# Performance work log

Measured on AMD Instinct MI355X. Metric: run time of the kernel, lower is better.

## Reference

```python
import jax, jax.numpy as jnp
from jax import lax
import numpy as np

BIG = jnp.float32(1e6)  # 'no feature in this column' sentinel distance


def setup_inputs() -> dict:
    key = jax.random.key(0)
    k1, k2 = jax.random.split(key)
    # Binary segmentation masks in {0,1}; surf() only uses astype(bool), i.e. != 0.
    pred = (jax.random.uniform(k1, (512, 512)) > 0.5).astype(jnp.float32)
    gt = (jax.random.uniform(k2, (512, 512)) > 0.5).astype(jnp.float32)
    return {"pred": pred, "gt": gt}


def _erode(x):
    # scipy binary_erosion with connectivity-1 (cross) structure, border_value=0:
    # pixel survives iff it and its 4 neighbors are all True (out-of-bounds = False).
    p = jnp.pad(x, 1, constant_values=False)
    return x & p[:-2, 1:-1] & p[2:, 1:-1] & p[1:-1, :-2] & p[1:-1, 2:]


def _edt(feat):
    # Exact Euclidean distance from every pixel to the nearest True pixel of `feat`.
    # Equals scipy distance_transform_edt(~feat) in the original code.
    H, W = feat.shape
    # --- pass 1: per-column 1D distance |r - k| to nearest feature (two sweeps) ---
    def sweep(carry, row):
        c = jnp.where(row, jnp.float32(0.0), carry + jnp.float32(1.0))
        return c, c
    init = jnp.full((W,), BIG, dtype=jnp.float32)
    _, df = lax.scan(sweep, init, feat)          # distance to nearest feature above
    _, db = lax.scan(sweep, init, feat[::-1])    # ... below
    g = jnp.minimum(df, db[::-1])                # [H, W] vertical distance
    g2 = g * g
    # --- pass 2: row-wise min-plus over column offsets (exact, separable) ---
    j = jnp.arange(W, dtype=jnp.float32)
    delta2 = (j[:, None] - j[None, :]) ** 2      # [W(c), W(j)]
    # D[r, c] = min_j ( g2[r, j] + (c - j)^2 )   -> [H, W, W] intermediate
    d2 = jnp.min(g2[:, None, :] + delta2[None, :, :], axis=-1)
    return jnp.sqrt(d2)


def reference(pred, gt):
    p = pred != 0
    g = gt != 0
    # Surface = mask minus its erosion
    S = p & ~_erode(p)
    Sprime = g & ~_erode(g)
    dta = _edt(S)       # distance field to pred surface (== edt(~S))
    dtb = _edt(Sprime)  # distance field to gt surface
    sm = S.astype(jnp.float32)
    spm = Sprime.astype(jnp.float32)
    # mean of concat(dta[Sprime], dtb[S]) without dynamic shapes
    num = jnp.sum(dta * spm) + jnp.sum(dtb * sm)
    den = jnp.sum(spm) + jnp.sum(sm)
    return num / den
```

## Files before the change

### kernel.cpp

```cpp
#include <hip/hip_runtime.h>

#define HH 512
#define WW 512
#define NPIX (HH*WW)

__global__ __launch_bounds__(256) void surf_kernel(
        const float* __restrict__ pred, const float* __restrict__ gt,
        unsigned char* __restrict__ mAB, unsigned int* __restrict__ ticket) {
    int idx4 = blockIdx.x * 256 + threadIdx.x;
    if (idx4 == 0) { *ticket = 0u; }
    if (idx4 >= NPIX / 4) return;
    int r  = idx4 >> 7;
    int c4 = (idx4 & 127) << 2;

    unsigned char bits[4] = {0, 0, 0, 0};
    const float* srcs[2] = { pred, gt };
    #pragma unroll
    for (int f = 0; f < 2; ++f) {
        const float* x = srcs[f];
        float4 v = ((const float4*)x)[idx4];
        float4 u = (r > 0)      ? ((const float4*)x)[idx4 - 128] : make_float4(0,0,0,0);
        float4 d = (r < HH - 1) ? ((const float4*)x)[idx4 + 128] : make_float4(0,0,0,0);
        float lS = (c4 > 0)        ? x[r * WW + c4 - 1] : 0.0f;
        float rS = (c4 + 4 < WW)   ? x[r * WW + c4 + 4] : 0.0f;
        float vv[4] = { v.x, v.y, v.z, v.w };
        float uu[4] = { u.x, u.y, u.z, u.w };
        float dd[4] = { d.x, d.y, d.z, d.w };
        #pragma unroll
        for (int e = 0; e < 4; ++e) {
            int c = c4 + e;
            bool ctr = vv[e] != 0.0f;
            bool up  = (r > 0)      && (uu[e] != 0.0f);
            bool dn  = (r < HH - 1) && (dd[e] != 0.0f);
            bool lf  = (c > 0)      && ((e == 0 ? lS : vv[e - 1]) != 0.0f);
            bool rt  = (c < WW - 1) && ((e == 3 ? rS : vv[e + 1]) != 0.0f);
            if (ctr && !(up && dn && lf && rt)) bits[e] |= (1 << f);
        }
    }
    uchar4 out;
    out.x = bits[0]; out.y = bits[1]; out.z = bits[2]; out.w = bits[3];
    ((uchar4*)mAB)[idx4] = out;
}

__global__ __launch_bounds__(512) void edt_kernel(
        const unsigned char* __restrict__ mAB,
        double* __restrict__ partials, unsigned int* __restrict__ ticket,
        float* __restrict__ out) {
    __shared__ float2 s2[WW];
    __shared__ double lred[16];
    __shared__ int winner;
    int r = blockIdx.x;
    int c = threadIdx.x;

    unsigned int own = mAB[r * WW + c];
    bool fa = (own & 1u) != 0u;
    bool fb = (own & 2u) != 0u;

    int foundA = fa ? 0 : -1;
    int foundB = fb ? 0 : -1;
    for (int kb = 1; kb < HH && (foundA < 0 || foundB < 0); kb += 4) {
        unsigned int mu[4], md[4];
        #pragma unroll
        for (int i = 0; i < 4; ++i) {
            int ku = kb + i;
            int ru = r - ku, rd = r + ku;
            mu[i] = (ru >= 0) ? (unsigned int)mAB[ru * WW + c] : 0u;
            md[i] = (rd < HH) ? (unsigned int)mAB[rd * WW + c] : 0u;
        }
        #pragma unroll
        for (int i = 0; i < 4; ++i) {
            unsigned int hit = mu[i] | md[i];
            if (foundA < 0 && (hit & 1u)) foundA = kb + i;
            if (foundB < 0 && (hit & 2u)) foundB = kb + i;
        }
    }
    float sent = 1e6f + (float)((r + 1 < HH - r) ? (r + 1) : (HH - r));
    float ga = (foundA >= 0) ? (float)foundA : sent;
    float gb = (foundB >= 0) ? (float)foundB : sent;
    s2[c] = make_float2(ga * ga, gb * gb);
    __syncthreads();

    float2 o2 = s2[c];
    float besta = o2.x, bestb = o2.y;
    for (int kb = 1; kb < WW; kb += 4) {
        float kk2 = (float)(kb * kb);
        if (kk2 >= besta && kk2 >= bestb) break;
        #pragma unroll
        for (int i = 0; i < 4; ++i) {
            int k = kb + i;
            float k2 = (float)(k * k);
            int cl = c - k, cr = c + k;
            if (cl >= 0) {
                float2 g = s2[cl];
                besta = fminf(besta, g.x + k2);
                bestb = fminf(bestb, g.y + k2);
            }
            if (cr < WW) {
                float2 g = s2[cr];
                besta = fminf(besta, g.x + k2);
                bestb = fminf(bestb, g.y + k2);
            }
        }
    }

    float wA = fa ? 1.0f : 0.0f;
    float wB = fb ? 1.0f : 0.0f;
    double lnum = (double)(sqrtf(besta) * wB + sqrtf(bestb) * wA);
    double lden = (double)(wA + wB);
    for (int off = 32; off > 0; off >>= 1) {
        lnum += __shfl_down(lnum, off, 64);
        lden += __shfl_down(lden, off, 64);
    }
    int wv = c >> 6;
    if ((c & 63) == 0) { lred[wv] = lnum; lred[8 + wv] = lden; }
    __syncthreads();
    if (c == 0) {
        double n = 0.0, d = 0.0;
        #pragma unroll
        for (int i = 0; i < 8; ++i) { n += lred[i]; d += lred[8 + i]; }
        partials[2 * r]     = n;
        partials[2 * r + 1] = d;
        __threadfence();
        unsigned int old = atomicAdd(ticket, 1u);
        winner = (old == HH - 1) ? 1 : 0;
    }
    __syncthreads();

    if (winner) {
        __threadfence();
        double n = partials[2 * c];
        double d = partials[2 * c + 1];
        for (int off = 32; off > 0; off >>= 1) {
            n += __shfl_down(n, off, 64);
            d += __shfl_down(d, off, 64);
        }
        if ((c & 63) == 0) { lred[c >> 6] = n; lred[8 + (c >> 6)] = d; }
        __syncthreads();
        if (c == 0) {
            double nn = 0.0, dd = 0.0;
            #pragma unroll
            for (int i = 0; i < 8; ++i) { nn += lred[i]; dd += lred[8 + i]; }
            out[0] = (float)(nn / dd);
        }
    }
}

extern "C" void kernel_launch(void* const* d_in, const int* in_sizes, int n_in,
                              void* d_out, int out_size, void* d_ws, size_t ws_size,
                              hipStream_t stream) {
    const float* pred = (const float*)d_in[0];
    const float* gt   = (const float*)d_in[1];
    float* out = (float*)d_out;

    char* ws = (char*)d_ws;
    unsigned int* tick = (unsigned int*)ws;
    double* partials   = (double*)(ws + 256);
    unsigned char* mAB = (unsigned char*)(ws + 256 + 8192);

    surf_kernel<<<NPIX / 4 / 256, 256, 0, stream>>>(pred, gt, mAB, tick);
    edt_kernel<<<HH, 512, 0, stream>>>(mAB, partials, tick, out);
}
```

Before: 71.97 us.

## Fuse surface and EDT kernels into one cooperative launch with grid barrier

Merges the surface-extraction kernel and the EDT/reduction kernel into a single cooperative kernel. A software grid barrier built on global atomics and a generation counter separates the two phases. Each block now stages three rows of both masks in shared memory to compute its row's surface bits, and keeps its own bits in registers instead of reloading them. This removes one kernel launch and the gap between launches, at the cost of a spin-wait barrier across 512 blocks and co-residency requirements.

```diff
diff --git a/kernel.cpp b/kernel.cpp
--- a/kernel.cpp
+++ b/kernel.cpp
@@ -2,60 +2,70 @@
 
 #define HH 512
 #define WW 512
-#define NPIX (HH*WW)
+#define NB HH
 
-__global__ __launch_bounds__(256) void surf_kernel(
+__device__ unsigned int g_cnt    = 0;
+__device__ unsigned int g_gen    = 0;
+__device__ unsigned int g_ticket = 0;
+
+__device__ __forceinline__ void grid_sync() {
+    __syncthreads();
+    if (threadIdx.x == 0) {
+        __threadfence();
+        unsigned int gen = __hip_atomic_load(&g_gen, __ATOMIC_RELAXED,
+                                             __HIP_MEMORY_SCOPE_AGENT);
+        unsigned int old = __hip_atomic_fetch_add(&g_cnt, 1u, __ATOMIC_ACQ_REL,
+                                                  __HIP_MEMORY_SCOPE_AGENT);
+        if (old == NB - 1u) {
+            __hip_atomic_store(&g_cnt, 0u, __ATOMIC_RELAXED,
+                               __HIP_MEMORY_SCOPE_AGENT);
+            __hip_atomic_fetch_add(&g_gen, 1u, __ATOMIC_RELEASE,
+                                   __HIP_MEMORY_SCOPE_AGENT);
+        } else {
+            while (__hip_atomic_load(&g_gen, __ATOMIC_RELAXED,
+                                     __HIP_MEMORY_SCOPE_AGENT) == gen) {
+                __builtin_amdgcn_s_sleep(1);
+            }
+        }
+        __threadfence();
+    }
+    __syncthreads();
+}
+
+__global__ __launch_bounds__(512, 4) void fused_kernel(
         const float* __restrict__ pred, const float* __restrict__ gt,
-        unsigned char* __restrict__ mAB, unsigned int* __restrict__ ticket) {
-    int idx4 = blockIdx.x * 256 + threadIdx.x;
-    if (idx4 == 0) { *ticket = 0u; }
-    if (idx4 >= NPIX / 4) return;
-    int r  = idx4 >> 7;
-    int c4 = (idx4 & 127) << 2;
+        unsigned char* __restrict__ mAB, double* __restrict__ partials,
+        float* __restrict__ out) {
+    __shared__ float  srow[2][3][WW];
+    __shared__ float2 s2[WW];
+    __shared__ double lred[16];
+    __shared__ int    winner;
+    const int r = blockIdx.x;
+    const int c = threadIdx.x;
 
-    unsigned char bits[4] = {0, 0, 0, 0};
-    const float* srcs[2] = { pred, gt };
+    srow[0][1][c] = pred[r * WW + c];
+    srow[1][1][c] = gt[r * WW + c];
+    srow[0][0][c] = (r > 0)      ? pred[(r - 1) * WW + c] : 0.0f;
+    srow[1][0][c] = (r > 0)      ? gt[(r - 1) * WW + c]   : 0.0f;
+    srow[0][2][c] = (r < HH - 1) ? pred[(r + 1) * WW + c] : 0.0f;
+    srow[1][2][c] = (r < HH - 1) ? gt[(r + 1) * WW + c]   : 0.0f;
+    __syncthreads();
+    unsigned int bits = 0u;
     #pragma unroll
     for (int f = 0; f < 2; ++f) {
-        const float* x = srcs[f];
-        float4 v = ((const float4*)x)[idx4];
-        float4 u = (r > 0)      ? ((const float4*)x)[idx4 - 128] : make_float4(0,0,0,0);
-        float4 d = (r < HH - 1) ? ((const float4*)x)[idx4 + 128] : make_float4(0,0,0,0);
-        float lS = (c4 > 0)        ? x[r * WW + c4 - 1] : 0.0f;
-        float rS = (c4 + 4 < WW)   ? x[r * WW + c4 + 4] : 0.0f;
-        float vv[4] = { v.x, v.y, v.z, v.w };
-        float uu[4] = { u.x, u.y, u.z, u.w };
-        float dd[4] = { d.x, d.y, d.z, d.w };
-        #pragma unroll
-        for (int e = 0; e < 4; ++e) {
-            int c = c4 + e;
-            bool ctr = vv[e] != 0.0f;
-            bool up  = (r > 0)      && (uu[e] != 0.0f);
-            bool dn  = (r < HH - 1) && (dd[e] != 0.0f);
-            bool lf  = (c > 0)      && ((e == 0 ? lS : vv[e - 1]) != 0.0f);
-            bool rt  = (c < WW - 1) && ((e == 3 ? rS : vv[e + 1]) != 0.0f);
-            if (ctr && !(up && dn && lf && rt)) bits[e] |= (1 << f);
-        }
+        bool ctr = srow[f][1][c] != 0.0f;
+        bool up  = srow[f][0][c] != 0.0f;
+        bool dn  = srow[f][2][c] != 0.0f;
+        bool lf  = (c > 0)      && (srow[f][1][c - 1] != 0.0f);
+        bool rt  = (c < WW - 1) && (srow[f][1][c + 1] != 0.0f);
+        if (ctr && !(up && dn && lf && rt)) bits |= (1u << f);
     }
-    uchar4 out;
-    out.x = bits[0]; out.y = bits[1]; out.z = bits[2]; out.w = bits[3];
-    ((uchar4*)mAB)[idx4] = out;
-}
+    mAB[r * WW + c] = (unsigned char)bits;
 
-__global__ __launch_bounds__(512) void edt_kernel(
-        const unsigned char* __restrict__ mAB,
-        double* __restrict__ partials, unsigned int* __restrict__ ticket,
-        float* __restrict__ out) {
-    __shared__ float2 s2[WW];
-    __shared__ double lred[16];
-    __shared__ int winner;
-    int r = blockIdx.x;
-    int c = threadIdx.x;
+    grid_sync();
 
-    unsigned int own = mAB[r * WW + c];
-    bool fa = (own & 1u) != 0u;
-    bool fb = (own & 2u) != 0u;
-
+    bool fa = (bits & 1u) != 0u;
+    bool fb = (bits & 2u) != 0u;
     int foundA = fa ? 0 : -1;
     int foundB = fb ? 0 : -1;
     for (int kb = 1; kb < HH && (foundA < 0 || foundB < 0); kb += 4) {
@@ -121,8 +131,9 @@
         partials[2 * r]     = n;
         partials[2 * r + 1] = d;
         __threadfence();
-        unsigned int old = atomicAdd(ticket, 1u);
-        winner = (old == HH - 1) ? 1 : 0;
+        unsigned int old = __hip_atomic_fetch_add(&g_ticket, 1u, __ATOMIC_ACQ_REL,
+                                                  __HIP_MEMORY_SCOPE_AGENT);
+        winner = (old == NB - 1u) ? 1 : 0;
     }
     __syncthreads();
 
@@ -141,6 +152,8 @@
             #pragma unroll
             for (int i = 0; i < 8; ++i) { nn += lred[i]; dd += lred[8 + i]; }
             out[0] = (float)(nn / dd);
+            __hip_atomic_store(&g_ticket, 0u, __ATOMIC_RELAXED,
+                               __HIP_MEMORY_SCOPE_AGENT);
         }
     }
 }
@@ -153,10 +166,11 @@
     float* out = (float*)d_out;
 
     char* ws = (char*)d_ws;
-    unsigned int* tick = (unsigned int*)ws;
-    double* partials   = (double*)(ws + 256);
-    unsigned char* mAB = (unsigned char*)(ws + 256 + 8192);
+    double* partials   = (double*)ws;
+    unsigned char* mAB = (unsigned char*)(ws + 8192);
 
-    surf_kernel<<<NPIX / 4 / 256, 256, 0, stream>>>(pred, gt, mAB, tick);
-    edt_kernel<<<HH, 512, 0, stream>>>(mAB, partials, tick, out);
+    void* args[] = { (void*)&pred, (void*)&gt, (void*)&mAB,
+                     (void*)&partials, (void*)&out };
+    hipLaunchCooperativeKernel((const void*)fused_kernel, dim3(NB), dim3(WW),
+                               args, 0, stream);
 }
```

Result: slower. 140.2 us (+94.9%).
